# Kernel optimization log

Hardware: AMD Instinct MI355X
Metric: run time of the kernel (lower is better)

The kernel has to match this reference:

```python
import jax, jax.numpy as jnp
import numpy as np

CLASSES_WEIGHT = jnp.array([1.0, 1.0, 1.0], dtype=jnp.float32)  # default for num_classes==3
EPS = 0.0001


def setup_inputs() -> dict:
    key = jax.random.key(0)
    k1, k2 = jax.random.split(key)
    B, C = 4096, 3
    source = jax.random.normal(k1, (B, C), dtype=jnp.float32)
    target = jax.random.randint(k2, (B,), 0, C, dtype=jnp.int64)
    return {"source": source, "target": target}


def reference(source, target):
    B, C = source.shape
    n2 = B * B
    # new_target = clamp(one_hot, 1e-4, 1.0) * classes_weight (weights are 1.0)
    T = jnp.clip(jax.nn.one_hot(target, C, dtype=jnp.float32), EPS, 1.0)
    T = T * CLASSES_WEIGHT[None, :]
    # new_source = softmax(logits)
    S = jax.nn.softmax(source, axis=1)
    LS = jnp.log(S)
    LT = jnp.log(T)
    sS = jnp.sum(S * LS, axis=-1)  # [B] sum_c s_ic log s_ic
    sT = jnp.sum(T * LT, axis=-1)  # [B]
    # L0: mean cross-entropy of new_target against softmax probs
    loss_0 = jnp.mean(-jnp.sum(T * LS, axis=-1))
    # L1: a_ij = -sum s_i (log s_j - log s_i) = sS_i - S_i . LS_j ; same for target
    A1 = sS[:, None] - S @ LS.T  # [B,B]
    B1 = sT[:, None] - T @ LT.T
    loss_1 = (EPS + jnp.sum(jnp.abs(A1 - B1))) / n2
    # L2: a_ij = -sum t_j (log s_i - log t_j) = sT_j - LS_i . T_j
    A2 = sT[None, :] - LS @ T.T
    B2 = sT[None, :] - LT @ T.T
    loss_2 = (EPS + jnp.sum(jnp.abs(A2 - B2))) / n2
    # L3: a_ij = sS_i - S_i . LS_j (== A1); b_ij = sT_i - T_i . LS_j
    B3 = sT[:, None] - T @ LS.T
    loss_3 = (EPS + jnp.sum(jnp.abs(A1 - B3))) / n2
    total = (loss_0 + loss_1) + (loss_2 + loss_3)
    return total, loss_0, loss_1, loss_2, loss_3
```

## Files before the change

kernel.cpp:

```cpp
#include <hip/hip_runtime.h>
#include <math.h>

#define BN   4096
#define GX   16
#define GY   32
#define TJ   128
#define NB   (GX * GY)

#define LOGE  (-9.210340371976184f)
#define EPSF  (1e-4f)
#define STC   (2.0f * EPSF * LOGE)

typedef float f32x2 __attribute__((ext_vector_type(2)));
__device__ __forceinline__ f32x2 sp(float v) { return (f32x2){v, v}; }

__global__ __launch_bounds__(256) void k_pairs(const float* __restrict__ src,
                                               const int* __restrict__ tgt,
                                               float* __restrict__ partial) {
    __shared__ float Lxs[TJ], Lys[TJ], Lzs[TJ];
    __shared__ int   sc[3], off[3], rk[3];
    __shared__ float4 wred[4];
    int tid = threadIdx.x;
    int bx = blockIdx.x, by = blockIdx.y;

    if (tid < 3) { sc[tid] = 0; rk[tid] = 0; }

    int i = bx * 256 + tid;
    float nS0, nS1, nS2, aI, sumLS_i, L0i, L1i, L2i;
    int ti;
    {
        float x0 = src[3*i], x1 = src[3*i+1], x2 = src[3*i+2];
        float m  = fmaxf(x0, fmaxf(x1, x2));
        float e0 = expf(x0 - m), e1 = expf(x1 - m), e2 = expf(x2 - m);
        float s  = e0 + e1 + e2;
        float inv = 1.0f / s;
        float S0 = e0 * inv, S1 = e1 * inv, S2 = e2 * inv;
        float ls = logf(s);
        L0i = x0 - m - ls; L1i = x1 - m - ls; L2i = x2 - m - ls;
        sumLS_i = L0i + L1i + L2i;
        float sS = S0 * L0i + S1 * L1i + S2 * L2i;
        ti = tgt[i];
        aI = sS - STC;
        nS0 = -S0; nS1 = -S1; nS2 = -S2;
    }
    float cSame = 2.0f * EPSF * LOGE;
    float cDiff = (1.0f + EPSF) * LOGE;
    float w0 = EPSF + ((ti == 0) ? (1.0f - EPSF) : 0.0f);
    float w1 = EPSF + ((ti == 1) ? (1.0f - EPSF) : 0.0f);
    float w2 = EPSF + ((ti == 2) ? (1.0f - EPSF) : 0.0f);
    float base = EPSF * (2.0f * LOGE - sumLS_i);
    float au0 = fabsf(base + (1.0f - EPSF) * (((ti == 0) ? 0.f : LOGE) - L0i));
    float au1 = fabsf(base + (1.0f - EPSF) * (((ti == 1) ? 0.f : LOGE) - L1i));
    float au2 = fabsf(base + (1.0f - EPSF) * (((ti == 2) ? 0.f : LOGE) - L2i));
    float LSt = (ti == 0) ? L0i : ((ti == 1) ? L1i : L2i);
    float c0 = (by == 0) ? -(EPSF * sumLS_i + (1.0f - EPSF) * LSt) : 0.0f;

    __syncthreads();

    int tj = -1;
    float jL0 = 0.f, jL1 = 0.f, jL2 = 0.f;
    if (tid < TJ) {
        int j = by * TJ + tid;
        float x0 = src[3*j], x1 = src[3*j+1], x2 = src[3*j+2];
        float m  = fmaxf(x0, fmaxf(x1, x2));
        float e0 = expf(x0 - m), e1 = expf(x1 - m), e2 = expf(x2 - m);
        float s  = e0 + e1 + e2;
        float ls = logf(s);
        jL0 = x0 - m - ls; jL1 = x1 - m - ls; jL2 = x2 - m - ls;
        tj = tgt[j];
        atomicAdd(&sc[tj], 1);
    }
    __syncthreads();
    if (tid == 0) { off[0] = 0; off[1] = sc[0]; off[2] = sc[0] + sc[1]; }
    __syncthreads();
    if (tid < TJ) {
        int r = atomicAdd(&rk[tj], 1);
        int pos = off[tj] + r;
        Lxs[pos] = jL0; Lys[pos] = jL1; Lzs[pos] = jL2;
    }
    __syncthreads();

    float c2 = (float)sc[0] * au0 + (float)sc[1] * au1 + (float)sc[2] * au2;

    f32x2 nS0v = sp(nS0), nS1v = sp(nS1), nS2v = sp(nS2), aIv = sp(aI);
    f32x2 w0v = sp(w0), w1v = sp(w1), w2v = sp(w2);
    f32x2 acc1v = sp(0.f), acc3v = sp(0.f);
    float a1s = 0.f, a3s = 0.f;

    const float4* Lx4 = reinterpret_cast<const float4*>(Lxs);
    const float4* Ly4 = reinterpret_cast<const float4*>(Lys);
    const float4* Lz4 = reinterpret_cast<const float4*>(Lzs);

    for (int s = 0; s < 3; ++s) {
        int k   = off[s];
        int end = k + sc[s];
        float cseg = (s == ti) ? cSame : cDiff;
        f32x2 cv = sp(cseg);
        while (k < end && (k & 3)) {
            float g = fmaf(nS0, Lxs[k], fmaf(nS1, Lys[k], fmaf(nS2, Lzs[k], aI)));
            a1s += fabsf(g + cseg);
            a3s += fabsf(fmaf(w0, Lxs[k], fmaf(w1, Lys[k], fmaf(w2, Lzs[k], g))));
            ++k;
        }
        #pragma unroll 2
        while (k + 3 < end) {
            int p = k >> 2;
            float4 qx = Lx4[p], qy = Ly4[p], qz = Lz4[p];
            f32x2 lx, ly, lz, g, t, e;
            lx = (f32x2){qx.x, qx.y}; ly = (f32x2){qy.x, qy.y}; lz = (f32x2){qz.x, qz.y};
            g = __builtin_elementwise_fma(nS2v, lz, aIv);
            g = __builtin_elementwise_fma(nS1v, ly, g);
            g = __builtin_elementwise_fma(nS0v, lx, g);
            t = g + cv;
            acc1v += __builtin_elementwise_max(t, -t);
            e = __builtin_elementwise_fma(w2v, lz, g);
            e = __builtin_elementwise_fma(w1v, ly, e);
            e = __builtin_elementwise_fma(w0v, lx, e);
            acc3v += __builtin_elementwise_max(e, -e);
            lx = (f32x2){qx.z, qx.w}; ly = (f32x2){qy.z, qy.w}; lz = (f32x2){qz.z, qz.w};
            g = __builtin_elementwise_fma(nS2v, lz, aIv);
            g = __builtin_elementwise_fma(nS1v, ly, g);
            g = __builtin_elementwise_fma(nS0v, lx, g);
            t = g + cv;
            acc1v += __builtin_elementwise_max(t, -t);
            e = __builtin_elementwise_fma(w2v, lz, g);
            e = __builtin_elementwise_fma(w1v, ly, e);
            e = __builtin_elementwise_fma(w0v, lx, e);
            acc3v += __builtin_elementwise_max(e, -e);
            k += 4;
        }
        while (k < end) {
            float g = fmaf(nS0, Lxs[k], fmaf(nS1, Lys[k], fmaf(nS2, Lzs[k], aI)));
            a1s += fabsf(g + cseg);
            a3s += fabsf(fmaf(w0, Lxs[k], fmaf(w1, Lys[k], fmaf(w2, Lzs[k], g))));
            ++k;
        }
    }
    float a1 = acc1v.x + acc1v.y + a1s;
    float a3 = acc3v.x + acc3v.y + a3s;

    for (int o = 32; o > 0; o >>= 1) {
        a1 += __shfl_down(a1, o);
        a3 += __shfl_down(a3, o);
        c2 += __shfl_down(c2, o);
        c0 += __shfl_down(c0, o);
    }
    int lane = tid & 63, wid = tid >> 6;
    if (lane == 0) wred[wid] = make_float4(a1, a3, c2, c0);
    __syncthreads();
    if (tid == 0) {
        float4 p = wred[0];
        #pragma unroll
        for (int w = 1; w < 4; ++w) {
            p.x += wred[w].x; p.y += wred[w].y;
            p.z += wred[w].z; p.w += wred[w].w;
        }
        int bid = by * GX + bx;
        *reinterpret_cast<float4*>(partial + bid * 4) = p;
    }
}

__global__ __launch_bounds__(512) void k_final(const float* __restrict__ partial,
                                               float* __restrict__ out) {
    __shared__ double s1[512], s3[512], s2[512], s0[512];
    int tid = threadIdx.x;
    float4 p = *reinterpret_cast<const float4*>(partial + tid * 4);
    s1[tid] = (double)p.x; s3[tid] = (double)p.y;
    s2[tid] = (double)p.z; s0[tid] = (double)p.w;
    __syncthreads();
    for (int s = 256; s > 0; s >>= 1) {
        if (tid < s) {
            s1[tid] += s1[tid + s]; s3[tid] += s3[tid + s];
            s2[tid] += s2[tid + s]; s0[tid] += s0[tid + s];
        }
        __syncthreads();
    }
    if (tid == 0) {
        double n2 = (double)BN * (double)BN;
        double l0 = s0[0] / (double)BN;
        double l1 = (1e-4 + s1[0]) / n2;
        double l2 = (1e-4 + s2[0]) / n2;
        double l3 = (1e-4 + s3[0]) / n2;
        out[0] = (float)((l0 + l1) + (l2 + l3));
        out[1] = (float)l0;
        out[2] = (float)l1;
        out[3] = (float)l2;
        out[4] = (float)l3;
    }
}

extern "C" void kernel_launch(void* const* d_in, const int* in_sizes, int n_in,
                              void* d_out, int out_size, void* d_ws, size_t ws_size,
                              hipStream_t stream) {
    const float* src = (const float*)d_in[0];
    const int*   tgt = (const int*)d_in[1];
    float*       out = (float*)d_out;
    float*   partial = (float*)d_ws;

    k_pairs<<<dim3(GX, GY), 256, 0, stream>>>(src, tgt, partial);
    k_final<<<1, 512, 0, stream>>>(partial, out);
}
```

Before: 14.75 us.

## Pad class segments to float4, decouple L3 FMA chain, shrink final reduction

```diff
diff --git a/kernel.cpp b/kernel.cpp
--- a/kernel.cpp
+++ b/kernel.cpp
@@ -5,6 +5,7 @@
 #define GX   16
 #define GY   32
 #define TJ   128
+#define TJP  144
 #define NB   (GX * GY)
 
 #define LOGE  (-9.210340371976184f)
@@ -17,13 +18,14 @@
 __global__ __launch_bounds__(256) void k_pairs(const float* __restrict__ src,
                                                const int* __restrict__ tgt,
                                                float* __restrict__ partial) {
-    __shared__ float Lxs[TJ], Lys[TJ], Lzs[TJ];
+    __shared__ float Lxs[TJP], Lys[TJP], Lzs[TJP];
     __shared__ int   sc[3], off[3], rk[3];
     __shared__ float4 wred[4];
     int tid = threadIdx.x;
     int bx = blockIdx.x, by = blockIdx.y;
 
     if (tid < 3) { sc[tid] = 0; rk[tid] = 0; }
+    if (tid < TJP) { Lxs[tid] = 0.f; Lys[tid] = 0.f; Lzs[tid] = 0.f; }
 
     int i = bx * 256 + tid;
     float nS0, nS1, nS2, aI, sumLS_i, L0i, L1i, L2i;
@@ -45,9 +47,9 @@
     }
     float cSame = 2.0f * EPSF * LOGE;
     float cDiff = (1.0f + EPSF) * LOGE;
-    float w0 = EPSF + ((ti == 0) ? (1.0f - EPSF) : 0.0f);
-    float w1 = EPSF + ((ti == 1) ? (1.0f - EPSF) : 0.0f);
-    float w2 = EPSF + ((ti == 2) ? (1.0f - EPSF) : 0.0f);
+    float dw0 = EPSF + ((ti == 0) ? (1.0f - EPSF) : 0.0f) + nS0;
+    float dw1 = EPSF + ((ti == 1) ? (1.0f - EPSF) : 0.0f) + nS1;
+    float dw2 = EPSF + ((ti == 2) ? (1.0f - EPSF) : 0.0f) + nS2;
     float base = EPSF * (2.0f * LOGE - sumLS_i);
     float au0 = fabsf(base + (1.0f - EPSF) * (((ti == 0) ? 0.f : LOGE) - L0i));
     float au1 = fabsf(base + (1.0f - EPSF) * (((ti == 1) ? 0.f : LOGE) - L1i));
@@ -71,7 +73,11 @@
         atomicAdd(&sc[tj], 1);
     }
     __syncthreads();
-    if (tid == 0) { off[0] = 0; off[1] = sc[0]; off[2] = sc[0] + sc[1]; }
+    if (tid == 0) {
+        off[0] = 0;
+        off[1] = (sc[0] + 3) & ~3;
+        off[2] = off[1] + ((sc[1] + 3) & ~3);
+    }
     __syncthreads();
     if (tid < TJ) {
         int r = atomicAdd(&rk[tj], 1);
@@ -82,62 +88,52 @@
 
     float c2 = (float)sc[0] * au0 + (float)sc[1] * au1 + (float)sc[2] * au2;
 
-    f32x2 nS0v = sp(nS0), nS1v = sp(nS1), nS2v = sp(nS2), aIv = sp(aI);
-    f32x2 w0v = sp(w0), w1v = sp(w1), w2v = sp(w2);
+    f32x2 nS0v = sp(nS0), nS1v = sp(nS1), nS2v = sp(nS2);
+    f32x2 dw0v = sp(dw0), dw1v = sp(dw1), dw2v = sp(dw2);
+    f32x2 aIv = sp(aI);
     f32x2 acc1v = sp(0.f), acc3v = sp(0.f);
-    float a1s = 0.f, a3s = 0.f;
+    float a1corr = 0.f;
+    int padtot = 0;
 
     const float4* Lx4 = reinterpret_cast<const float4*>(Lxs);
     const float4* Ly4 = reinterpret_cast<const float4*>(Lys);
     const float4* Lz4 = reinterpret_cast<const float4*>(Lzs);
 
     for (int s = 0; s < 3; ++s) {
-        int k   = off[s];
-        int end = k + sc[s];
-        float cseg = (s == ti) ? cSame : cDiff;
-        f32x2 cv = sp(cseg);
-        while (k < end && (k & 3)) {
-            float g = fmaf(nS0, Lxs[k], fmaf(nS1, Lys[k], fmaf(nS2, Lzs[k], aI)));
-            a1s += fabsf(g + cseg);
-            a3s += fabsf(fmaf(w0, Lxs[k], fmaf(w1, Lys[k], fmaf(w2, Lzs[k], g))));
-            ++k;
-        }
+        int cnt = sc[s];
+        int len = (cnt + 3) & ~3;
+        float aIc = aI + ((s == ti) ? cSame : cDiff);
+        f32x2 av1 = sp(aIc);
+        int p0 = off[s] >> 2, p1 = (off[s] + len) >> 2;
         #pragma unroll 2
-        while (k + 3 < end) {
-            int p = k >> 2;
+        for (int p = p0; p < p1; ++p) {
             float4 qx = Lx4[p], qy = Ly4[p], qz = Lz4[p];
-            f32x2 lx, ly, lz, g, t, e;
+            f32x2 lx, ly, lz, t, e;
             lx = (f32x2){qx.x, qx.y}; ly = (f32x2){qy.x, qy.y}; lz = (f32x2){qz.x, qz.y};
-            g = __builtin_elementwise_fma(nS2v, lz, aIv);
-            g = __builtin_elementwise_fma(nS1v, ly, g);
-            g = __builtin_elementwise_fma(nS0v, lx, g);
-            t = g + cv;
+            t = __builtin_elementwise_fma(nS2v, lz, av1);
+            t = __builtin_elementwise_fma(nS1v, ly, t);
+            t = __builtin_elementwise_fma(nS0v, lx, t);
             acc1v += __builtin_elementwise_max(t, -t);
-            e = __builtin_elementwise_fma(w2v, lz, g);
-            e = __builtin_elementwise_fma(w1v, ly, e);
-            e = __builtin_elementwise_fma(w0v, lx, e);
+            e = __builtin_elementwise_fma(dw2v, lz, aIv);
+            e = __builtin_elementwise_fma(dw1v, ly, e);
+            e = __builtin_elementwise_fma(dw0v, lx, e);
             acc3v += __builtin_elementwise_max(e, -e);
             lx = (f32x2){qx.z, qx.w}; ly = (f32x2){qy.z, qy.w}; lz = (f32x2){qz.z, qz.w};
-            g = __builtin_elementwise_fma(nS2v, lz, aIv);
-            g = __builtin_elementwise_fma(nS1v, ly, g);
-            g = __builtin_elementwise_fma(nS0v, lx, g);
-            t = g + cv;
+            t = __builtin_elementwise_fma(nS2v, lz, av1);
+            t = __builtin_elementwise_fma(nS1v, ly, t);
+            t = __builtin_elementwise_fma(nS0v, lx, t);
             acc1v += __builtin_elementwise_max(t, -t);
-            e = __builtin_elementwise_fma(w2v, lz, g);
-            e = __builtin_elementwise_fma(w1v, ly, e);
-            e = __builtin_elementwise_fma(w0v, lx, e);
+            e = __builtin_elementwise_fma(dw2v, lz, aIv);
+            e = __builtin_elementwise_fma(dw1v, ly, e);
+            e = __builtin_elementwise_fma(dw0v, lx, e);
             acc3v += __builtin_elementwise_max(e, -e);
-            k += 4;
         }
-        while (k < end) {
-            float g = fmaf(nS0, Lxs[k], fmaf(nS1, Lys[k], fmaf(nS2, Lzs[k], aI)));
-            a1s += fabsf(g + cseg);
-            a3s += fabsf(fmaf(w0, Lxs[k], fmaf(w1, Lys[k], fmaf(w2, Lzs[k], g))));
-            ++k;
-        }
+        int pad = len - cnt;
+        a1corr += (float)pad * fabsf(aIc);
+        padtot += pad;
     }
-    float a1 = acc1v.x + acc1v.y + a1s;
-    float a3 = acc3v.x + acc3v.y + a3s;
+    float a1 = acc1v.x + acc1v.y - a1corr;
+    float a3 = acc3v.x + acc3v.y - (float)padtot * fabsf(aI);
 
     for (int o = 32; o > 0; o >>= 1) {
         a1 += __shfl_down(a1, o);
@@ -160,27 +156,28 @@
     }
 }
 
-__global__ __launch_bounds__(512) void k_final(const float* __restrict__ partial,
-                                               float* __restrict__ out) {
-    __shared__ double s1[512], s3[512], s2[512], s0[512];
-    int tid = threadIdx.x;
-    float4 p = *reinterpret_cast<const float4*>(partial + tid * 4);
-    s1[tid] = (double)p.x; s3[tid] = (double)p.y;
-    s2[tid] = (double)p.z; s0[tid] = (double)p.w;
-    __syncthreads();
-    for (int s = 256; s > 0; s >>= 1) {
-        if (tid < s) {
-            s1[tid] += s1[tid + s]; s3[tid] += s3[tid + s];
-            s2[tid] += s2[tid + s]; s0[tid] += s0[tid + s];
-        }
-        __syncthreads();
+__global__ __launch_bounds__(64) void k_final(const float* __restrict__ partial,
+                                              float* __restrict__ out) {
+    int lane = threadIdx.x;
+    double s1 = 0, s3 = 0, s2 = 0, s0 = 0;
+    #pragma unroll
+    for (int p = lane; p < NB; p += 64) {
+        float4 v = reinterpret_cast<const float4*>(partial)[p];
+        s1 += (double)v.x; s3 += (double)v.y;
+        s2 += (double)v.z; s0 += (double)v.w;
     }
-    if (tid == 0) {
+    for (int o = 32; o > 0; o >>= 1) {
+        s1 += __shfl_down(s1, o);
+        s3 += __shfl_down(s3, o);
+        s2 += __shfl_down(s2, o);
+        s0 += __shfl_down(s0, o);
+    }
+    if (lane == 0) {
         double n2 = (double)BN * (double)BN;
-        double l0 = s0[0] / (double)BN;
-        double l1 = (1e-4 + s1[0]) / n2;
-        double l2 = (1e-4 + s2[0]) / n2;
-        double l3 = (1e-4 + s3[0]) / n2;
+        double l0 = s0 / (double)BN;
+        double l1 = (1e-4 + s1) / n2;
+        double l2 = (1e-4 + s2) / n2;
+        double l3 = (1e-4 + s3) / n2;
         out[0] = (float)((l0 + l1) + (l2 + l3));
         out[1] = (float)l0;
         out[2] = (float)l1;
@@ -198,5 +195,5 @@
     float*   partial = (float*)d_ws;
 
     k_pairs<<<dim3(GX, GY), 256, 0, stream>>>(src, tgt, partial);
-    k_final<<<1, 512, 0, stream>>>(partial, out);
+    k_final<<<1, 64, 0, stream>>>(partial, out);
 }
```

Result: slower. 15.89 us (+7.7%).
